# Performance work log

Measured on AMD Instinct MI355X. Metric: run time of the kernel, lower is better.

The kernel has to match this reference:

```python
import jax, jax.numpy as jnp
import numpy as np

KERNEL_NUM = 21
SIGMA = 0.1
EXACT_SIGMA = 0.001

def _kernel_params(k=KERNEL_NUM, sigma=SIGMA, exact_sigma=EXACT_SIGMA):
    step = 1.0 / (k - 1)
    left = -1.0 + step
    right = 1.0 - step
    mu = np.hstack([np.arange(left, right, (right - left) / (k - 2)), right, 1.0])
    sig = np.where(mu == 1.0, exact_sigma, sigma)
    return jnp.asarray(mu, jnp.float32), jnp.asarray(sig, jnp.float32)

MU, SIG = _kernel_params()

def setup_inputs() -> dict:
    key = jax.random.key(0)
    ks = jax.random.split(key, 11)
    B, LQ, LD, V, E = 1024, 20, 200, 100000, 128
    return {
        "q1": jax.random.randint(ks[0], (B, LQ), 0, V),
        "d1": jax.random.randint(ks[1], (B, LD), 0, V),
        "q2": jax.random.randint(ks[2], (B, LQ), 0, V),
        "d2": jax.random.randint(ks[3], (B, LD), 0, V),
        "emb": jax.random.normal(ks[4], (V, E), jnp.float32),
        "W1": jax.random.normal(ks[5], (10, 21), jnp.float32) * 0.1,
        "b1": jax.random.normal(ks[6], (10,), jnp.float32) * 0.1,
        "W2": jax.random.normal(ks[7], (5, 10), jnp.float32) * 0.1,
        "b2": jax.random.normal(ks[8], (5,), jnp.float32) * 0.1,
        "W3": jax.random.normal(ks[9], (1, 5), jnp.float32) * 0.1,
        "b3": jax.random.normal(ks[10], (1,), jnp.float32) * 0.1,
    }

def _matching_matrix(emb, q_ids, d_ids, alpha=1e-6):
    q = emb[q_ids]  # [B,LQ,E]
    d = emb[d_ids]  # [B,LD,E]
    nom = jnp.einsum('bqe,bde->bqd', q, d)
    qn = jnp.sqrt(jnp.sum(q * q, axis=2) + alpha)  # [B,LQ]
    dn = jnp.sqrt(jnp.sum(d * d, axis=2) + alpha)  # [B,LD]
    return nom / (qn[:, :, None] * dn[:, None, :])  # [B,LQ,LD]

def _apply_kernels(M):
    # M: [B,LQ,LD] -> phi: [B,LQ,LD,K]
    phi = jnp.exp(-jnp.square(M[..., None] - MU) / (2.0 * SIG * SIG))
    return jnp.sum(jnp.log1p(jnp.sum(phi, axis=2)), axis=1)  # [B,K]

def _mlp(x, W1, b1, W2, b2, W3, b3):
    x = jax.nn.relu(x)
    x = x @ W1.T + b1
    x = jax.nn.relu(x)
    x = x @ W2.T + b2
    x = jax.nn.relu(x)
    return x @ W3.T + b3  # [B,1]

def _predict(emb, q, d, W1, b1, W2, b2, W3, b3):
    M = _matching_matrix(emb, q, d)
    k = _apply_kernels(M)
    return _mlp(k, W1, b1, W2, b2, W3, b3)

def reference(q1, d1, q2, d2, emb, W1, b1, W2, b2, W3, b3):
    l1 = _predict(emb, q1, d1, W1, b1, W2, b2, W3, b3)
    l2 = _predict(emb, q2, d2, W1, b1, W2, b2, W3, b3)
    return jax.nn.sigmoid(l1 - l2)  # [B,1]
```

## Files before the change

### kernel.cpp

```cpp
#include <hip/hip_runtime.h>
#include <hip/hip_bf16.h>

#define NB 1024
#define LQ 20
#define LD 200
#define E4 32
#define NK 21
#define NTILE 13

typedef __attribute__((ext_vector_type(8))) short bf16x8;
typedef __attribute__((ext_vector_type(4))) float f32x4;
typedef __attribute__((ext_vector_type(2))) float f32x2;

__device__ __forceinline__ unsigned cvt2(float lo, float hi) {
    __hip_bfloat162 h = __float22bfloat162_rn(make_float2(lo, hi));
    unsigned u;
    __builtin_memcpy(&u, &h, 4);
    return u;
}

__device__ __forceinline__ bf16x8 pack8(float4 f0, float4 f1) {
    union { unsigned u[4]; bf16x8 v; } r;
    r.u[0] = cvt2(f0.x, f0.y);
    r.u[1] = cvt2(f0.z, f0.w);
    r.u[2] = cvt2(f1.x, f1.y);
    r.u[3] = cvt2(f1.z, f1.w);
    return r.v;
}

__device__ __forceinline__ float sq8(float4 f0, float4 f1, float s) {
    s = fmaf(f0.x, f0.x, s); s = fmaf(f0.y, f0.y, s);
    s = fmaf(f0.z, f0.z, s); s = fmaf(f0.w, f0.w, s);
    s = fmaf(f1.x, f1.x, s); s = fmaf(f1.y, f1.y, s);
    s = fmaf(f1.z, f1.z, s); s = fmaf(f1.w, f1.w, s);
    return s;
}

__device__ __forceinline__ float fast_exp2(float x) {
#if __has_builtin(__builtin_amdgcn_exp2f)
    return __builtin_amdgcn_exp2f(x);
#else
    return __expf(x * 0.69314718056f);
#endif
}

#define DN0 0.60653066f
#define DN1 0.13533528f
#define DN2 1.1108997e-2f
#define DN3 3.3546263e-4f
#define DN4 3.7266532e-6f
#define DN5 1.5229979e-8f
#define DN6 2.2897348e-11f
#define DN7 1.2664166e-14f
#define DN8 2.5767912e-18f
#define DN9 1.9287498e-22f

__device__ __forceinline__ f32x2 pk_exp2(f32x2 a) {
    f32x2 r; r.x = fast_exp2(a.x); r.y = fast_exp2(a.y); return r;
}

__device__ __forceinline__ void rbf2(f32x2 m, f32x2* S) {
    const float DN[10] = {DN0, DN1, DN2, DN3, DN4, DN5, DN6, DN7, DN8, DN9};
    const f32x2 x = m - 0.05f;
    const f32x2 p = pk_exp2(x * x * -72.13475204f);
    S[10] += p;
    f32x2 w = pk_exp2(x * 14.4269504089f);
    f32x2 q = p;
    #pragma unroll
    for (int n = 1; n <= 9; ++n) {
        q = q * w;
        S[10 + n] = __builtin_elementwise_fma(q, (f32x2)(DN[n - 1]), S[10 + n]);
    }
    w = pk_exp2(x * -14.4269504089f);
    q = p;
    #pragma unroll
    for (int n = 1; n <= 10; ++n) {
        q = q * w;
        S[10 - n] = __builtin_elementwise_fma(q, (f32x2)(DN[n - 1]), S[10 - n]);
    }
    const f32x2 d = m - 1.0f;
    S[20] += pk_exp2(d * d * -721347.5204f);
}

__device__ __forceinline__ void rbf1(float m, float* S) {
    const float DN[10] = {DN0, DN1, DN2, DN3, DN4, DN5, DN6, DN7, DN8, DN9};
    const float x = m - 0.05f;
    const float p = fast_exp2(x * x * -72.13475204f);
    S[10] += p;
    float w = fast_exp2(x * 14.4269504089f);
    float q = p;
    #pragma unroll
    for (int n = 1; n <= 9; ++n) {
        q *= w;
        S[10 + n] = fmaf(q, DN[n - 1], S[10 + n]);
    }
    w = fast_exp2(x * -14.4269504089f);
    q = p;
    #pragma unroll
    for (int n = 1; n <= 10; ++n) {
        q *= w;
        S[10 - n] = fmaf(q, DN[n - 1], S[10 - n]);
    }
    const float d = m - 1.0f;
    S[20] += fast_exp2(d * d * -721347.5204f);
}

__global__ __launch_bounds__(256, 2) void knrm_main(
    const int* __restrict__ q1, const int* __restrict__ d1,
    const int* __restrict__ q2, const int* __restrict__ d2,
    const float* __restrict__ emb,
    const float* __restrict__ W1, const float* __restrict__ b1,
    const float* __restrict__ W2, const float* __restrict__ b2,
    const float* __restrict__ W3, const float* __restrict__ b3,
    float* __restrict__ out)
{
    __shared__ float sPhiW[4][LQ][NK];
    __shared__ float sX[2][NK];
    __shared__ float sH1[2][10];
    __shared__ float sH2[2][5];

    const int b    = blockIdx.x;
    const int t    = threadIdx.x;
    const int lane = t & 63, wave = t >> 6;
    const int pred = wave >> 1, wv = wave & 1;
    const int c    = lane & 15, quad = lane >> 4;
    const int* __restrict__ qi = pred ? q2 : q1;
    const int* __restrict__ di = pred ? d2 : d1;
    const float4* emb4 = (const float4*)emb;

    const int qid0 = qi[b * LQ + c];
    const int r1   = 16 + c;
    const int qid1 = qi[b * LQ + (r1 < LQ ? r1 : LQ - 1)];
    int tile = wv;
    const int j0 = tile * 16 + c;
    const int id0 = di[b * LD + (j0 < LD ? j0 : LD - 1)];
    int idn;
    {
        const int jn = j0 + 32;
        idn = di[b * LD + (jn < LD ? jn : LD - 1)];
    }

    float4 ld0, ld1, ld2, ld3, ld4, ld5, ld6, ld7;
    {
        const float4* db = emb4 + (size_t)(unsigned)id0 * E4;
        ld0 = db[quad * 2];      ld1 = db[quad * 2 + 1];
        ld2 = db[8 + quad * 2];  ld3 = db[8 + quad * 2 + 1];
        ld4 = db[16 + quad * 2]; ld5 = db[16 + quad * 2 + 1];
        ld6 = db[24 + quad * 2]; ld7 = db[24 + quad * 2 + 1];
    }

    bf16x8 aF[2][4];
    float rqA, rqB;
    {
        const float4* qb0 = emb4 + (size_t)(unsigned)qid0 * E4;
        const float4* qb1 = emb4 + (size_t)(unsigned)qid1 * E4;
        float qs0 = 0.f, qs1 = 0.f;
        #pragma unroll
        for (int ks = 0; ks < 4; ++ks) {
            float4 f0 = qb0[ks * 8 + quad * 2];
            float4 f1 = qb0[ks * 8 + quad * 2 + 1];
            qs0 = sq8(f0, f1, qs0);
            aF[0][ks] = pack8(f0, f1);
            float4 g0 = qb1[ks * 8 + quad * 2];
            float4 g1 = qb1[ks * 8 + quad * 2 + 1];
            qs1 = sq8(g0, g1, qs1);
            aF[1][ks] = pack8(g0, g1);
        }
        if (c >= LQ - 16) {
            #pragma unroll
            for (int ks = 0; ks < 4; ++ks) aF[1][ks] = (bf16x8)0;
            qs1 = 0.f;
        }
        qs0 += __shfl_xor(qs0, 16); qs0 += __shfl_xor(qs0, 32);
        qs1 += __shfl_xor(qs1, 16); qs1 += __shfl_xor(qs1, 32);
        rqA = rsqrtf(qs0 + 1e-6f);
        rqB = rsqrtf(qs1 + 1e-6f);
    }

    f32x2 Sp[NK];
    float S1[NK];
    #pragma unroll
    for (int k = 0; k < NK; ++k) { Sp[k] = (f32x2)(0.f); S1[k] = 0.f; }

    #pragma unroll 1
    while (true) {
        if (tile == NTILE - 1 && c >= (LD - (NTILE - 1) * 16)) {
            ld0 = ld1 = ld2 = ld3 = ld4 = ld5 = ld6 = ld7 = make_float4(0.f, 0.f, 0.f, 0.f);
        }

        float dsq = 0.f;
        f32x4 acc0 = {0.f, 0.f, 0.f, 0.f};
        f32x4 acc1 = {0.f, 0.f, 0.f, 0.f};
        {
            dsq = sq8(ld0, ld1, dsq);
            bf16x8 bFk = pack8(ld0, ld1);
            acc0 = __builtin_amdgcn_mfma_f32_16x16x32_bf16(bFk, aF[0][0], acc0, 0, 0, 0);
            acc1 = __builtin_amdgcn_mfma_f32_16x16x32_bf16(bFk, aF[1][0], acc1, 0, 0, 0);
        }
        {
            dsq = sq8(ld2, ld3, dsq);
            bf16x8 bFk = pack8(ld2, ld3);
            acc0 = __builtin_amdgcn_mfma_f32_16x16x32_bf16(bFk, aF[0][1], acc0, 0, 0, 0);
            acc1 = __builtin_amdgcn_mfma_f32_16x16x32_bf16(bFk, aF[1][1], acc1, 0, 0, 0);
        }
        {
            dsq = sq8(ld4, ld5, dsq);
            bf16x8 bFk = pack8(ld4, ld5);
            acc0 = __builtin_amdgcn_mfma_f32_16x16x32_bf16(bFk, aF[0][2], acc0, 0, 0, 0);
            acc1 = __builtin_amdgcn_mfma_f32_16x16x32_bf16(bFk, aF[1][2], acc1, 0, 0, 0);
        }
        {
            dsq = sq8(ld6, ld7, dsq);
            bf16x8 bFk = pack8(ld6, ld7);
            acc0 = __builtin_amdgcn_mfma_f32_16x16x32_bf16(bFk, aF[0][3], acc0, 0, 0, 0);
            acc1 = __builtin_amdgcn_mfma_f32_16x16x32_bf16(bFk, aF[1][3], acc1, 0, 0, 0);
        }

        const int ntile = tile + 2;
        if (ntile < NTILE) {
            const float4* db = emb4 + (size_t)(unsigned)idn * E4;
            ld0 = db[quad * 2];      ld1 = db[quad * 2 + 1];
            ld2 = db[8 + quad * 2];  ld3 = db[8 + quad * 2 + 1];
            ld4 = db[16 + quad * 2]; ld5 = db[16 + quad * 2 + 1];
            ld6 = db[24 + quad * 2]; ld7 = db[24 + quad * 2 + 1];
            if (ntile + 2 < NTILE) {
                const int jn2 = (ntile + 2) * 16 + c;
                idn = di[b * LD + (jn2 < LD ? jn2 : LD - 1)];
            }
        }

        dsq += __shfl_xor(dsq, 16);
        dsq += __shfl_xor(dsq, 32);
        const float rdc = rsqrtf(dsq + 1e-6f);
        float rdv[4];
        #pragma unroll
        for (int r = 0; r < 4; ++r) rdv[r] = __shfl(rdc, quad * 4 + r);

        f32x2 ma, mb;
        ma.x = acc0[0] * rdv[0] * rqA;
        ma.y = acc0[1] * rdv[1] * rqA;
        mb.x = acc0[2] * rdv[2] * rqA;
        mb.y = acc0[3] * rdv[3] * rqA;
        rbf2(ma, Sp);
        rbf2(mb, Sp);

        float m1[4];
        #pragma unroll
        for (int r = 0; r < 4; ++r) m1[r] = acc1[r] * rdv[r] * rqB;
        const int src = (lane & 48) | ((lane >> 2) & 3);
        const float g0 = __shfl(m1[0], src);
        const float g1 = __shfl(m1[1], src);
        const float g2 = __shfl(m1[2], src);
        const float g3 = __shfl(m1[3], src);
        const int rsel = lane & 3;
        const float mv = (rsel == 0) ? g0 : (rsel == 1) ? g1 : (rsel == 2) ? g2 : g3;
        rbf1(mv, S1);

        tile += 2;
        if (tile >= NTILE) break;
    }

    float S0f[NK];
    #pragma unroll
    for (int k = 0; k < NK; ++k) {
        float s0 = Sp[k].x + Sp[k].y;
        s0 += __shfl_xor(s0, 16);
        s0 += __shfl_xor(s0, 32);
        S0f[k] = s0;
        S1[k] += __shfl_xor(S1[k], 1);
        S1[k] += __shfl_xor(S1[k], 2);
        S1[k] += __shfl_xor(S1[k], 16);
        S1[k] += __shfl_xor(S1[k], 32);
    }
    if (quad == 0) {
        #pragma unroll
        for (int k = 0; k < NK; ++k) sPhiW[wave][c][k] = S0f[k];
    }
    if ((lane & 51) == 0) {
        #pragma unroll
        for (int k = 0; k < NK; ++k) sPhiW[wave][16 + (lane >> 2)][k] = S1[k];
    }
    __syncthreads();

    const int ew = t >> 6, et = t & 63;

    if (ew < 2 && et < NK) {
        const float mu_t = 0.1f * (float)et - 0.95f;
        const float pad  = (et < 20) ? 8.0f * fast_exp2(-72.13475204f * mu_t * mu_t) : 0.0f;
        float s = 0.f;
        #pragma unroll
        for (int i = 0; i < LQ; ++i) {
            const float v = sPhiW[2 * ew][i][et] + sPhiW[2 * ew + 1][i][et] - pad;
            s += __logf(1.0f + v);
        }
        sX[ew][et] = fmaxf(s, 0.f);
    }
    __syncthreads();

    if (ew < 2 && et < 10) {
        float v = b1[et];
        #pragma unroll
        for (int k = 0; k < NK; ++k) v += W1[et * NK + k] * sX[ew][k];
        sH1[ew][et] = fmaxf(v, 0.f);
    }
    __syncthreads();

    if (ew < 2 && et < 5) {
        float v = b2[et];
        #pragma unroll
        for (int k = 0; k < 10; ++k) v += W2[et * 10 + k] * sH1[ew][k];
        sH2[ew][et] = fmaxf(v, 0.f);
    }
    __syncthreads();

    if (t == 0) {
        float l0 = b3[0], l1 = b3[0];
        #pragma unroll
        for (int k = 0; k < 5; ++k) {
            l0 += W3[k] * sH2[0][k];
            l1 += W3[k] * sH2[1][k];
        }
        out[b] = 1.0f / (1.0f + __expf(l1 - l0));
    }
}

extern "C" void kernel_launch(void* const* d_in, const int* in_sizes, int n_in,
                              void* d_out, int out_size, void* d_ws, size_t ws_size,
                              hipStream_t stream) {
    knrm_main<<<NB, 256, 0, stream>>>(
        (const int*)d_in[0], (const int*)d_in[1],
        (const int*)d_in[2], (const int*)d_in[3],
        (const float*)d_in[4],
        (const float*)d_in[5], (const float*)d_in[6],
        (const float*)d_in[7], (const float*)d_in[8],
        (const float*)d_in[9], (const float*)d_in[10],
        (float*)d_out);
}
```

Baseline: 137.1 us.

## Unroll tile loop, defer tail-row RBF into packed pairs, skip exact kernel when unneeded

Fully unrolls the document tile loop. The scalar RBF work for the extra four query rows is deferred: the values are kept in a small array and processed afterwards in packed pairs, with a dummy value filling unused slots. The exact-match kernel for the main rows is now computed only when some lane in the wave has a similarity above 0.98. Squared norms are accumulated with packed two-wide FMAs. These changes cut VALU and exp work, at the cost of more registers from the unroll and a wave-uniform branch that diverges only rarely.

```diff
diff --git a/kernel.cpp b/kernel.cpp
--- a/kernel.cpp
+++ b/kernel.cpp
@@ -7,6 +7,7 @@
 #define E4 32
 #define NK 21
 #define NTILE 13
+#define MDUMMY 3.0f
 
 typedef __attribute__((ext_vector_type(8))) short bf16x8;
 typedef __attribute__((ext_vector_type(4))) float f32x4;
@@ -28,11 +29,15 @@
     return r.v;
 }
 
-__device__ __forceinline__ float sq8(float4 f0, float4 f1, float s) {
-    s = fmaf(f0.x, f0.x, s); s = fmaf(f0.y, f0.y, s);
-    s = fmaf(f0.z, f0.z, s); s = fmaf(f0.w, f0.w, s);
-    s = fmaf(f1.x, f1.x, s); s = fmaf(f1.y, f1.y, s);
-    s = fmaf(f1.z, f1.z, s); s = fmaf(f1.w, f1.w, s);
+__device__ __forceinline__ f32x2 fma2(f32x2 a, f32x2 b, f32x2 c) {
+    return __builtin_elementwise_fma(a, b, c);
+}
+
+__device__ __forceinline__ f32x2 sqacc(float4 f0, float4 f1, f32x2 s) {
+    f32x2 a = {f0.x, f0.y}, b = {f0.z, f0.w};
+    f32x2 c = {f1.x, f1.y}, d = {f1.z, f1.w};
+    s = fma2(a, a, s); s = fma2(b, b, s);
+    s = fma2(c, c, s); s = fma2(d, d, s);
     return s;
 }
 
@@ -69,40 +74,15 @@
     #pragma unroll
     for (int n = 1; n <= 9; ++n) {
         q = q * w;
-        S[10 + n] = __builtin_elementwise_fma(q, (f32x2)(DN[n - 1]), S[10 + n]);
+        S[10 + n] = fma2(q, (f32x2)(DN[n - 1]), S[10 + n]);
     }
     w = pk_exp2(x * -14.4269504089f);
     q = p;
     #pragma unroll
     for (int n = 1; n <= 10; ++n) {
         q = q * w;
-        S[10 - n] = __builtin_elementwise_fma(q, (f32x2)(DN[n - 1]), S[10 - n]);
-    }
-    const f32x2 d = m - 1.0f;
-    S[20] += pk_exp2(d * d * -721347.5204f);
-}
-
-__device__ __forceinline__ void rbf1(float m, float* S) {
-    const float DN[10] = {DN0, DN1, DN2, DN3, DN4, DN5, DN6, DN7, DN8, DN9};
-    const float x = m - 0.05f;
-    const float p = fast_exp2(x * x * -72.13475204f);
-    S[10] += p;
-    float w = fast_exp2(x * 14.4269504089f);
-    float q = p;
-    #pragma unroll
-    for (int n = 1; n <= 9; ++n) {
-        q *= w;
-        S[10 + n] = fmaf(q, DN[n - 1], S[10 + n]);
-    }
-    w = fast_exp2(x * -14.4269504089f);
-    q = p;
-    #pragma unroll
-    for (int n = 1; n <= 10; ++n) {
-        q *= w;
-        S[10 - n] = fmaf(q, DN[n - 1], S[10 - n]);
-    }
-    const float d = m - 1.0f;
-    S[20] += fast_exp2(d * d * -721347.5204f);
+        S[10 - n] = fma2(q, (f32x2)(DN[n - 1]), S[10 - n]);
+    }
 }
 
 __global__ __launch_bounds__(256, 2) void knrm_main(
@@ -131,14 +111,9 @@
     const int qid0 = qi[b * LQ + c];
     const int r1   = 16 + c;
     const int qid1 = qi[b * LQ + (r1 < LQ ? r1 : LQ - 1)];
-    int tile = wv;
-    const int j0 = tile * 16 + c;
-    const int id0 = di[b * LD + (j0 < LD ? j0 : LD - 1)];
-    int idn;
-    {
-        const int jn = j0 + 32;
-        idn = di[b * LD + (jn < LD ? jn : LD - 1)];
-    }
+    const int j0   = wv * 16 + c;
+    const int id0  = di[b * LD + j0];
+    int idn = di[b * LD + j0 + 32];
 
     float4 ld0, ld1, ld2, ld3, ld4, ld5, ld6, ld7;
     {
@@ -154,18 +129,19 @@
     {
         const float4* qb0 = emb4 + (size_t)(unsigned)qid0 * E4;
         const float4* qb1 = emb4 + (size_t)(unsigned)qid1 * E4;
-        float qs0 = 0.f, qs1 = 0.f;
+        f32x2 q0 = {0.f, 0.f}, q1v = {0.f, 0.f};
         #pragma unroll
         for (int ks = 0; ks < 4; ++ks) {
             float4 f0 = qb0[ks * 8 + quad * 2];
             float4 f1 = qb0[ks * 8 + quad * 2 + 1];
-            qs0 = sq8(f0, f1, qs0);
+            q0 = sqacc(f0, f1, q0);
             aF[0][ks] = pack8(f0, f1);
             float4 g0 = qb1[ks * 8 + quad * 2];
             float4 g1 = qb1[ks * 8 + quad * 2 + 1];
-            qs1 = sq8(g0, g1, qs1);
+            q1v = sqacc(g0, g1, q1v);
             aF[1][ks] = pack8(g0, g1);
         }
+        float qs0 = q0.x + q0.y, qs1 = q1v.x + q1v.y;
         if (c >= LQ - 16) {
             #pragma unroll
             for (int ks = 0; ks < 4; ++ks) aF[1][ks] = (bf16x8)0;
@@ -178,99 +154,126 @@
     }
 
     f32x2 Sp[NK];
-    float S1[NK];
-    #pragma unroll
-    for (int k = 0; k < NK; ++k) { Sp[k] = (f32x2)(0.f); S1[k] = 0.f; }
-
-    #pragma unroll 1
-    while (true) {
-        if (tile == NTILE - 1 && c >= (LD - (NTILE - 1) * 16)) {
-            ld0 = ld1 = ld2 = ld3 = ld4 = ld5 = ld6 = ld7 = make_float4(0.f, 0.f, 0.f, 0.f);
-        }
-
-        float dsq = 0.f;
-        f32x4 acc0 = {0.f, 0.f, 0.f, 0.f};
-        f32x4 acc1 = {0.f, 0.f, 0.f, 0.f};
-        {
-            dsq = sq8(ld0, ld1, dsq);
-            bf16x8 bFk = pack8(ld0, ld1);
-            acc0 = __builtin_amdgcn_mfma_f32_16x16x32_bf16(bFk, aF[0][0], acc0, 0, 0, 0);
-            acc1 = __builtin_amdgcn_mfma_f32_16x16x32_bf16(bFk, aF[1][0], acc1, 0, 0, 0);
-        }
-        {
-            dsq = sq8(ld2, ld3, dsq);
-            bf16x8 bFk = pack8(ld2, ld3);
-            acc0 = __builtin_amdgcn_mfma_f32_16x16x32_bf16(bFk, aF[0][1], acc0, 0, 0, 0);
-            acc1 = __builtin_amdgcn_mfma_f32_16x16x32_bf16(bFk, aF[1][1], acc1, 0, 0, 0);
-        }
-        {
-            dsq = sq8(ld4, ld5, dsq);
-            bf16x8 bFk = pack8(ld4, ld5);
-            acc0 = __builtin_amdgcn_mfma_f32_16x16x32_bf16(bFk, aF[0][2], acc0, 0, 0, 0);
-            acc1 = __builtin_amdgcn_mfma_f32_16x16x32_bf16(bFk, aF[1][2], acc1, 0, 0, 0);
-        }
-        {
-            dsq = sq8(ld6, ld7, dsq);
-            bf16x8 bFk = pack8(ld6, ld7);
-            acc0 = __builtin_amdgcn_mfma_f32_16x16x32_bf16(bFk, aF[0][3], acc0, 0, 0, 0);
-            acc1 = __builtin_amdgcn_mfma_f32_16x16x32_bf16(bFk, aF[1][3], acc1, 0, 0, 0);
-        }
-
-        const int ntile = tile + 2;
-        if (ntile < NTILE) {
-            const float4* db = emb4 + (size_t)(unsigned)idn * E4;
-            ld0 = db[quad * 2];      ld1 = db[quad * 2 + 1];
-            ld2 = db[8 + quad * 2];  ld3 = db[8 + quad * 2 + 1];
-            ld4 = db[16 + quad * 2]; ld5 = db[16 + quad * 2 + 1];
-            ld6 = db[24 + quad * 2]; ld7 = db[24 + quad * 2 + 1];
-            if (ntile + 2 < NTILE) {
-                const int jn2 = (ntile + 2) * 16 + c;
-                idn = di[b * LD + (jn2 < LD ? jn2 : LD - 1)];
-            }
-        }
-
-        dsq += __shfl_xor(dsq, 16);
-        dsq += __shfl_xor(dsq, 32);
-        const float rdc = rsqrtf(dsq + 1e-6f);
-        float rdv[4];
-        #pragma unroll
-        for (int r = 0; r < 4; ++r) rdv[r] = __shfl(rdc, quad * 4 + r);
-
-        f32x2 ma, mb;
-        ma.x = acc0[0] * rdv[0] * rqA;
-        ma.y = acc0[1] * rdv[1] * rqA;
-        mb.x = acc0[2] * rdv[2] * rqA;
-        mb.y = acc0[3] * rdv[3] * rqA;
-        rbf2(ma, Sp);
-        rbf2(mb, Sp);
-
-        float m1[4];
-        #pragma unroll
-        for (int r = 0; r < 4; ++r) m1[r] = acc1[r] * rdv[r] * rqB;
-        const int src = (lane & 48) | ((lane >> 2) & 3);
-        const float g0 = __shfl(m1[0], src);
-        const float g1 = __shfl(m1[1], src);
-        const float g2 = __shfl(m1[2], src);
-        const float g3 = __shfl(m1[3], src);
-        const int rsel = lane & 3;
-        const float mv = (rsel == 0) ? g0 : (rsel == 1) ? g1 : (rsel == 2) ? g2 : g3;
-        rbf1(mv, S1);
-
-        tile += 2;
-        if (tile >= NTILE) break;
-    }
-
-    float S0f[NK];
+    #pragma unroll
+    for (int k = 0; k < NK; ++k) Sp[k] = (f32x2)(0.f);
+    float mv[8];
+    mv[7] = MDUMMY;
+
+    #pragma unroll
+    for (int ti = 0; ti < 7; ++ti) {
+        const int tile = wv + 2 * ti;
+        if (tile < NTILE) {
+            if (tile == NTILE - 1 && c >= (LD - (NTILE - 1) * 16)) {
+                ld0 = ld1 = ld2 = ld3 = ld4 = ld5 = ld6 = ld7 =
+                    make_float4(0.f, 0.f, 0.f, 0.f);
+            }
+
+            f32x2 dq = {0.f, 0.f};
+            f32x4 acc0 = {0.f, 0.f, 0.f, 0.f};
+            f32x4 acc1 = {0.f, 0.f, 0.f, 0.f};
+            {
+                dq = sqacc(ld0, ld1, dq);
+                bf16x8 bFk = pack8(ld0, ld1);
+                acc0 = __builtin_amdgcn_mfma_f32_16x16x32_bf16(bFk, aF[0][0], acc0, 0, 0, 0);
+                acc1 = __builtin_amdgcn_mfma_f32_16x16x32_bf16(bFk, aF[1][0], acc1, 0, 0, 0);
+            }
+            {
+                dq = sqacc(ld2, ld3, dq);
+                bf16x8 bFk = pack8(ld2, ld3);
+                acc0 = __builtin_amdgcn_mfma_f32_16x16x32_bf16(bFk, aF[0][1], acc0, 0, 0, 0);
+                acc1 = __builtin_amdgcn_mfma_f32_16x16x32_bf16(bFk, aF[1][1], acc1, 0, 0, 0);
+            }
+            {
+                dq = sqacc(ld4, ld5, dq);
+                bf16x8 bFk = pack8(ld4, ld5);
+                acc0 = __builtin_amdgcn_mfma_f32_16x16x32_bf16(bFk, aF[0][2], acc0, 0, 0, 0);
+                acc1 = __builtin_amdgcn_mfma_f32_16x16x32_bf16(bFk, aF[1][2], acc1, 0, 0, 0);
+            }
+            {
+                dq = sqacc(ld6, ld7, dq);
+                bf16x8 bFk = pack8(ld6, ld7);
+                acc0 = __builtin_amdgcn_mfma_f32_16x16x32_bf16(bFk, aF[0][3], acc0, 0, 0, 0);
+                acc1 = __builtin_amdgcn_mfma_f32_16x16x32_bf16(bFk, aF[1][3], acc1, 0, 0, 0);
+            }
+
+            const int ntile = tile + 2;
+            if (ntile < NTILE) {
+                const float4* db = emb4 + (size_t)(unsigned)idn * E4;
+                ld0 = db[quad * 2];      ld1 = db[quad * 2 + 1];
+                ld2 = db[8 + quad * 2];  ld3 = db[8 + quad * 2 + 1];
+                ld4 = db[16 + quad * 2]; ld5 = db[16 + quad * 2 + 1];
+                ld6 = db[24 + quad * 2]; ld7 = db[24 + quad * 2 + 1];
+                if (ntile + 2 < NTILE) {
+                    const int jn2 = (ntile + 2) * 16 + c;
+                    idn = di[b * LD + (jn2 < LD ? jn2 : LD - 1)];
+                }
+            }
+
+            float dsq = dq.x + dq.y;
+            dsq += __shfl_xor(dsq, 16);
+            dsq += __shfl_xor(dsq, 32);
+            const float rdc = rsqrtf(dsq + 1e-6f);
+            float rdv[4];
+            #pragma unroll
+            for (int r = 0; r < 4; ++r) rdv[r] = __shfl(rdc, quad * 4 + r);
+
+            const f32x2 r01 = {rdv[0], rdv[1]}, r23 = {rdv[2], rdv[3]};
+            f32x2 ma = {acc0[0], acc0[1]};
+            f32x2 mb = {acc0[2], acc0[3]};
+            ma = ma * r01 * rqA;
+            mb = mb * r23 * rqA;
+            rbf2(ma, Sp);
+            rbf2(mb, Sp);
+
+            const float mx = fmaxf(fmaxf(ma.x, ma.y), fmaxf(mb.x, mb.y));
+            if (__any(mx > 0.98f)) {
+                const f32x2 da = ma - 1.0f, db2 = mb - 1.0f;
+                Sp[20] += pk_exp2(da * da * -721347.5204f);
+                Sp[20] += pk_exp2(db2 * db2 * -721347.5204f);
+            }
+
+            f32x2 n01 = {acc1[0], acc1[1]};
+            f32x2 n23 = {acc1[2], acc1[3]};
+            n01 = n01 * r01 * rqB;
+            n23 = n23 * r23 * rqB;
+            const int src = (lane & 48) | ((lane >> 2) & 3);
+            const float g0 = __shfl(n01.x, src);
+            const float g1 = __shfl(n01.y, src);
+            const float g2 = __shfl(n23.x, src);
+            const float g3 = __shfl(n23.y, src);
+            const int rsel = lane & 3;
+            mv[ti] = (rsel == 0) ? g0 : (rsel == 1) ? g1 : (rsel == 2) ? g2 : g3;
+        } else {
+            mv[ti] = MDUMMY;
+        }
+    }
+
+    f32x2 S1p[NK];
+    #pragma unroll
+    for (int k = 0; k < NK; ++k) S1p[k] = (f32x2)(0.f);
+    #pragma unroll
+    for (int pp = 0; pp < 4; ++pp) {
+        f32x2 mm;
+        mm.x = mv[2 * pp];
+        mm.y = mv[2 * pp + 1];
+        rbf2(mm, S1p);
+        const f32x2 dd = mm - 1.0f;
+        S1p[20] += pk_exp2(dd * dd * -721347.5204f);
+    }
+
+    float S0f[NK], S1f[NK];
     #pragma unroll
     for (int k = 0; k < NK; ++k) {
         float s0 = Sp[k].x + Sp[k].y;
         s0 += __shfl_xor(s0, 16);
         s0 += __shfl_xor(s0, 32);
         S0f[k] = s0;
-        S1[k] += __shfl_xor(S1[k], 1);
-        S1[k] += __shfl_xor(S1[k], 2);
-        S1[k] += __shfl_xor(S1[k], 16);
-        S1[k] += __shfl_xor(S1[k], 32);
+        float s1 = S1p[k].x + S1p[k].y;
+        s1 += __shfl_xor(s1, 1);
+        s1 += __shfl_xor(s1, 2);
+        s1 += __shfl_xor(s1, 16);
+        s1 += __shfl_xor(s1, 32);
+        S1f[k] = s1;
     }
     if (quad == 0) {
         #pragma unroll
@@ -278,7 +281,7 @@
     }
     if ((lane & 51) == 0) {
         #pragma unroll
-        for (int k = 0; k < NK; ++k) sPhiW[wave][16 + (lane >> 2)][k] = S1[k];
+        for (int k = 0; k < NK; ++k) sPhiW[wave][16 + (lane >> 2)][k] = S1f[k];
     }
     __syncthreads();
 
```

Result: faster. 133.0 us, median of 2 (-3.0%).
